# Kernel optimization log

Measured on AMD Instinct MI355X. Metric: run time of the kernel, lower is better.

The kernel has to match this reference:

```python
import jax, jax.numpy as jnp
import numpy as np

B, T, C, H = 4, 2048, 1024, 16
D = C // H  # head dim = 64


def setup_inputs() -> dict:
    key = jax.random.key(0)
    k1, k2, k3 = jax.random.split(key, 3)
    scale = 0.02
    x = jax.random.normal(k1, (B, T, C), dtype=jnp.float32)
    Wqkv = jax.random.normal(k2, (C, 3 * C), dtype=jnp.float32) * scale
    bqkv = jnp.zeros((3 * C,), dtype=jnp.float32)
    Wproj = jax.random.normal(k3, (C, C), dtype=jnp.float32) * scale
    bproj = jnp.zeros((C,), dtype=jnp.float32)
    return {"x": x, "Wqkv": Wqkv, "bqkv": bqkv, "Wproj": Wproj, "bproj": bproj}


def reference(x, Wqkv, bqkv, Wproj, bproj):
    Bx, Tx, Cx = x.shape
    qkv = x @ Wqkv + bqkv  # [B,T,3C]
    q, k, v = jnp.split(qkv, 3, axis=2)
    # [B,T,C] -> [B,H,T,D]
    q = q.reshape(Bx, Tx, H, D).transpose(0, 2, 1, 3)
    k = k.reshape(Bx, Tx, H, D).transpose(0, 2, 1, 3)
    v = v.reshape(Bx, Tx, H, D).transpose(0, 2, 1, 3)
    scores = jnp.einsum('bhqd,bhkd->bhqk', q, k) * (D ** -0.5)
    causal = jnp.tril(jnp.ones((Tx, Tx), dtype=bool))
    scores = jnp.where(causal[None, None], scores, -jnp.inf)
    attn = jax.nn.softmax(scores, axis=-1)
    out = jnp.einsum('bhqk,bhkd->bhqd', attn, v)  # [B,H,T,D]
    out = out.transpose(0, 2, 1, 3).reshape(Bx, Tx, Cx)
    return out @ Wproj + bproj
```

## Files before the change

### kernel.cpp

```cpp
#include <hip/hip_runtime.h>
#include <stdint.h>

typedef __bf16 bf16x8 __attribute__((ext_vector_type(8)));
typedef float  f32x4  __attribute__((ext_vector_type(4)));
typedef short  s16x8  __attribute__((ext_vector_type(8)));

__device__ __forceinline__ unsigned short f2bf(float f) {
  unsigned u = __builtin_bit_cast(unsigned, f);
  u += 0x7fffu + ((u >> 16) & 1u);
  return (unsigned short)(u >> 16);
}

__device__ __forceinline__ bf16x8 ld8(const unsigned short* p) {
  return __builtin_bit_cast(bf16x8, *reinterpret_cast<const s16x8*>(p));
}

#define BB 4
#define TT 2048
#define CC 1024
#define HH 16
#define DD 64
#define MM (BB*TT)

__global__ __launch_bounds__(256) void cvt_f32_bf16(const float* __restrict__ in,
                                                    unsigned short* __restrict__ out, int n) {
  int idx = blockIdx.x * blockDim.x + threadIdx.x;
  int stride = gridDim.x * blockDim.x;
  for (int i = idx * 4; i < n; i += stride * 4) {
    float4 v = *reinterpret_cast<const float4*>(in + i);
    ushort4 o;
    o.x = f2bf(v.x); o.y = f2bf(v.y); o.z = f2bf(v.z); o.w = f2bf(v.w);
    *reinterpret_cast<ushort4*>(out + i) = o;
  }
}

__global__ __launch_bounds__(256) void transpose_cvt(const float* __restrict__ in,
                                                     unsigned short* __restrict__ out,
                                                     int K, int N) {
  __shared__ float tile[32][33];
  int kb = blockIdx.y * 32, nb = blockIdx.x * 32;
  int tx = threadIdx.x, ty = threadIdx.y;
  for (int i = 0; i < 4; i++)
    tile[ty + i*8][tx] = in[(size_t)(kb + ty + i*8) * N + nb + tx];
  __syncthreads();
  for (int i = 0; i < 4; i++)
    out[(size_t)(nb + ty + i*8) * K + kb + tx] = f2bf(tile[tx][ty + i*8]);
}

#define BMT 128
#define BNT 128
#define BKT 32
#define LDT 56

template<int EPI>
__global__ __launch_bounds__(256)
void gemm_bt(const unsigned short* __restrict__ A, const unsigned short* __restrict__ Bt,
             const float* __restrict__ bias, int K,
             unsigned short* __restrict__ qbuf, unsigned short* __restrict__ kbuf,
             unsigned short* __restrict__ vtbuf, float* __restrict__ outf)
{
  __shared__ unsigned short As[BMT * LDT];
  __shared__ unsigned short Bs[BNT * LDT];
  const int tid  = threadIdx.x;
  const int lane = tid & 63;
  const int w    = tid >> 6;
  const int wr   = w >> 1, wc = w & 1;
  const int lo   = lane & 15, hi = lane >> 4;
  const int row0 = blockIdx.x * BMT, col0 = blockIdx.y * BNT;

  f32x4 acc[4][4];
  for (int m = 0; m < 4; m++)
    for (int n = 0; n < 4; n++)
      for (int j = 0; j < 4; j++) acc[m][n][j] = 0.f;

  const int sr = tid >> 2;
  const int sc = (tid & 3) * 8;

  for (int k0 = 0; k0 < K; k0 += BKT) {
    s16x8 a0 = *reinterpret_cast<const s16x8*>(A  + (size_t)(row0 + sr)      * K + k0 + sc);
    s16x8 a1 = *reinterpret_cast<const s16x8*>(A  + (size_t)(row0 + sr + 64) * K + k0 + sc);
    s16x8 b0 = *reinterpret_cast<const s16x8*>(Bt + (size_t)(col0 + sr)      * K + k0 + sc);
    s16x8 b1 = *reinterpret_cast<const s16x8*>(Bt + (size_t)(col0 + sr + 64) * K + k0 + sc);
    *reinterpret_cast<s16x8*>(As + sr        * LDT + sc) = a0;
    *reinterpret_cast<s16x8*>(As + (sr + 64) * LDT + sc) = a1;
    *reinterpret_cast<s16x8*>(Bs + sr        * LDT + sc) = b0;
    *reinterpret_cast<s16x8*>(Bs + (sr + 64) * LDT + sc) = b1;
    __syncthreads();

    bf16x8 af[4], bfr[4];
    for (int m = 0; m < 4; m++)
      af[m] = __builtin_bit_cast(bf16x8,
        *reinterpret_cast<const s16x8*>(As + (wr*64 + m*16 + lo) * LDT + hi*8));
    for (int n = 0; n < 4; n++)
      bfr[n] = __builtin_bit_cast(bf16x8,
        *reinterpret_cast<const s16x8*>(Bs + (wc*64 + n*16 + lo) * LDT + hi*8));
    for (int m = 0; m < 4; m++)
      for (int n = 0; n < 4; n++)
        acc[m][n] = __builtin_amdgcn_mfma_f32_16x16x32_bf16(af[m], bfr[n], acc[m][n], 0, 0, 0);
    __syncthreads();
  }

  if (EPI == 0) {
    const int sec = col0 >> 10;
    for (int m = 0; m < 4; m++) {
      int rbase = row0 + wr*64 + m*16 + hi*4;
      for (int n = 0; n < 4; n++) {
        int c  = col0 + wc*64 + n*16 + lo;
        int cc = c & 1023;
        int h  = cc >> 6, d = cc & 63;
        float bv = bias[c];
        for (int i = 0; i < 4; i++) {
          int r = rbase + i;
          int b = r >> 11, t = r & 2047;
          int bh = b * HH + h;
          unsigned short val = f2bf(acc[m][n][i] + bv);
          if (sec == 0)      qbuf [((size_t)bh * TT + t) * DD + d] = val;
          else if (sec == 1) kbuf [((size_t)bh * TT + t) * DD + d] = val;
          else               vtbuf[((size_t)bh * DD + d) * TT + t] = val;
        }
      }
    }
  } else {
    for (int m = 0; m < 4; m++) {
      int rbase = row0 + wr*64 + m*16 + hi*4;
      for (int n = 0; n < 4; n++) {
        int c = col0 + wc*64 + n*16 + lo;
        float bv = bias[c];
        for (int i = 0; i < 4; i++)
          outf[(size_t)(rbase + i) * CC + c] = acc[m][n][i] + bv;
      }
    }
  }
}

#define PLD 88

__global__ __launch_bounds__(256)
void attn_kernel(const unsigned short* __restrict__ qbuf,
                 const unsigned short* __restrict__ kbuf,
                 const unsigned short* __restrict__ vtbuf,
                 unsigned short* __restrict__ obuf)
{
  __shared__ unsigned short P[4][32 * PLD];
  const int tid  = threadIdx.x;
  const int lane = tid & 63;
  const int w    = tid >> 6;
  const int lo   = lane & 15, hi = lane >> 4;
  const int bh   = blockIdx.x;
  const int qblk = gridDim.y - 1 - blockIdx.y;
  const int qbase = qblk * 128 + w * 32;

  bf16x8 aq[2][2];
  #pragma unroll
  for (int st = 0; st < 2; st++) {
    const unsigned short* qp = qbuf + ((size_t)bh * TT + qbase + st*16 + lo) * DD + hi * 8;
    aq[st][0] = ld8(qp);
    aq[st][1] = ld8(qp + 32);
  }

  float mrow[2][4], lrow[2][4];
  f32x4 acc_o[2][4];
  #pragma unroll
  for (int st = 0; st < 2; st++)
    for (int i = 0; i < 4; i++) {
      mrow[st][i] = -1e30f; lrow[st][i] = 0.f;
      for (int f = 0; f < 4; f++) acc_o[st][f][i] = 0.f;
    }

  unsigned short* Pw = &P[w][0];
  const int nfull = qbase >> 6;

  for (int kt = 0; kt <= nfull; ++kt) {
    const int kbase = kt * 64;
    const bool diag = (kt == nfull);

    f32x4 s[2][4];
    #pragma unroll
    for (int st = 0; st < 2; st++)
      for (int f = 0; f < 4; f++)
        for (int j = 0; j < 4; j++) s[st][f][j] = 0.f;

    __builtin_amdgcn_s_setprio(1);
    #pragma unroll
    for (int f = 0; f < 4; f++) {
      const unsigned short* kp = kbuf + ((size_t)bh * TT + kbase + f*16 + lo) * DD + hi * 8;
      bf16x8 b0 = ld8(kp);
      bf16x8 b1 = ld8(kp + 32);
      s[0][f] = __builtin_amdgcn_mfma_f32_16x16x32_bf16(aq[0][0], b0, s[0][f], 0, 0, 0);
      s[0][f] = __builtin_amdgcn_mfma_f32_16x16x32_bf16(aq[0][1], b1, s[0][f], 0, 0, 0);
      s[1][f] = __builtin_amdgcn_mfma_f32_16x16x32_bf16(aq[1][0], b0, s[1][f], 0, 0, 0);
      s[1][f] = __builtin_amdgcn_mfma_f32_16x16x32_bf16(aq[1][1], b1, s[1][f], 0, 0, 0);
    }
    __builtin_amdgcn_s_setprio(0);

    #pragma unroll
    for (int st = 0; st < 2; st++) {
      const int rowoff = qbase + st*16 + hi*4;
      float tm[4] = {-1e30f, -1e30f, -1e30f, -1e30f};
      #pragma unroll
      for (int f = 0; f < 4; f++)
        for (int i = 0; i < 4; i++) {
          float v = s[st][f][i] * 0.125f;
          if (diag && (kbase + f*16 + lo > rowoff + i)) v = -1e30f;
          s[st][f][i] = v;
          tm[i] = fmaxf(tm[i], v);
        }
      #pragma unroll
      for (int xm = 1; xm < 16; xm <<= 1)
        for (int i = 0; i < 4; i++) tm[i] = fmaxf(tm[i], __shfl_xor(tm[i], xm));
      float rs[4];
      #pragma unroll
      for (int i = 0; i < 4; i++) {
        float mn   = fmaxf(mrow[st][i], tm[i]);
        float corr = __expf(mrow[st][i] - mn);
        mrow[st][i] = mn;
        float r = 0.f;
        #pragma unroll
        for (int f = 0; f < 4; f++) {
          float p = __expf(s[st][f][i] - mn);
          r += p;
          Pw[(st*16 + hi*4 + i) * PLD + f*16 + lo] = f2bf(p);
        }
        rs[i] = r;
        lrow[st][i] *= corr;
        #pragma unroll
        for (int f = 0; f < 4; f++) acc_o[st][f][i] *= corr;
      }
      #pragma unroll
      for (int xm = 1; xm < 16; xm <<= 1)
        for (int i = 0; i < 4; i++) rs[i] += __shfl_xor(rs[i], xm);
      for (int i = 0; i < 4; i++) lrow[st][i] += rs[i];
    }

    bf16x8 pa[2][2];
    #pragma unroll
    for (int st = 0; st < 2; st++) {
      pa[st][0] = ld8(Pw + (st*16 + lo) * PLD + hi * 8);
      pa[st][1] = ld8(Pw + (st*16 + lo) * PLD + 32 + hi * 8);
    }
    __builtin_amdgcn_s_setprio(1);
    #pragma unroll
    for (int f = 0; f < 4; f++) {
      const unsigned short* vp = vtbuf + ((size_t)bh * DD + f*16 + lo) * TT + kbase + hi * 8;
      bf16x8 v0 = ld8(vp);
      bf16x8 v1 = ld8(vp + 32);
      acc_o[0][f] = __builtin_amdgcn_mfma_f32_16x16x32_bf16(pa[0][0], v0, acc_o[0][f], 0, 0, 0);
      acc_o[0][f] = __builtin_amdgcn_mfma_f32_16x16x32_bf16(pa[0][1], v1, acc_o[0][f], 0, 0, 0);
      acc_o[1][f] = __builtin_amdgcn_mfma_f32_16x16x32_bf16(pa[1][0], v0, acc_o[1][f], 0, 0, 0);
      acc_o[1][f] = __builtin_amdgcn_mfma_f32_16x16x32_bf16(pa[1][1], v1, acc_o[1][f], 0, 0, 0);
    }
    __builtin_amdgcn_s_setprio(0);
  }

  const int b = bh >> 4, h = bh & 15;
  #pragma unroll
  for (int st = 0; st < 2; st++)
    for (int f = 0; f < 4; f++)
      for (int i = 0; i < 4; i++) {
        int r = qbase + st*16 + hi*4 + i;
        float v = acc_o[st][f][i] / lrow[st][i];
        obuf[((size_t)(b * TT + r)) * CC + h*64 + f*16 + lo] = f2bf(v);
      }
}

extern "C" void kernel_launch(void* const* d_in, const int* in_sizes, int n_in,
                              void* d_out, int out_size, void* d_ws, size_t ws_size,
                              hipStream_t stream) {
  const float* x     = (const float*)d_in[0];
  const float* Wqkv  = (const float*)d_in[1];
  const float* bqkv  = (const float*)d_in[2];
  const float* Wproj = (const float*)d_in[3];
  const float* bproj = (const float*)d_in[4];
  float* out = (float*)d_out;

  unsigned short* ws  = (unsigned short*)d_ws;
  unsigned short* xb  = ws;
  unsigned short* w1t = xb  + (size_t)MM * CC;
  unsigned short* w2t = w1t + (size_t)3 * CC * CC;
  unsigned short* qbf = w2t + (size_t)CC * CC;
  unsigned short* kbf = qbf + (size_t)BB * HH * TT * DD;
  unsigned short* vtb = kbf + (size_t)BB * HH * TT * DD;
  unsigned short* obf = xb;

  cvt_f32_bf16<<<2048, 256, 0, stream>>>(x, xb, MM * CC);
  transpose_cvt<<<dim3(3*CC/32, CC/32), dim3(32, 8), 0, stream>>>(Wqkv, w1t, CC, 3*CC);
  transpose_cvt<<<dim3(CC/32,  CC/32), dim3(32, 8), 0, stream>>>(Wproj, w2t, CC, CC);

  gemm_bt<0><<<dim3(MM/BMT, 3*CC/BNT), 256, 0, stream>>>(xb, w1t, bqkv, CC,
                                                         qbf, kbf, vtb, nullptr);
  attn_kernel<<<dim3(BB*HH, TT/128), 256, 0, stream>>>(qbf, kbf, vtb, obf);
  gemm_bt<1><<<dim3(MM/BMT, CC/BNT), 256, 0, stream>>>(obf, w2t, bproj, CC,
                                                       nullptr, nullptr, nullptr, out);
}
```

Measured before the change: 371.3 us.

## Use direct global-to-LDS loads in GEMMs and software-pipeline attention QK with PV

The GEMM now loads tiles with global_load_lds straight into unpadded shared memory, skipping the register round-trip. The cost is possible LDS bank conflicts, since the stride drops from 56 to 32. The attention loop computes the next tile's QK scores before the current tile's PV, so score MFMAs overlap softmax and V loads, at the cost of more registers. Softmax folds log2(e) into the scale and uses exp2f instead of __expf.

```diff
diff --git a/kernel.cpp b/kernel.cpp
--- a/kernel.cpp
+++ b/kernel.cpp
@@ -14,6 +14,8 @@
 __device__ __forceinline__ bf16x8 ld8(const unsigned short* p) {
   return __builtin_bit_cast(bf16x8, *reinterpret_cast<const s16x8*>(p));
 }
+
+#define MFMA16(a,b,c) __builtin_amdgcn_mfma_f32_16x16x32_bf16((a),(b),(c),0,0,0)
 
 #define BB 4
 #define TT 2048
@@ -47,68 +49,74 @@
     out[(size_t)(nb + ty + i*8) * K + kb + tx] = f2bf(tile[tx][ty + i*8]);
 }
 
-#define BMT 128
-#define BNT 128
-#define BKT 32
-#define LDT 56
-
 template<int EPI>
 __global__ __launch_bounds__(256)
-void gemm_bt(const unsigned short* __restrict__ A, const unsigned short* __restrict__ Bt,
-             const float* __restrict__ bias, int K,
-             unsigned short* __restrict__ qbuf, unsigned short* __restrict__ kbuf,
-             unsigned short* __restrict__ vtbuf, float* __restrict__ outf)
+void gemm_glds(const unsigned short* __restrict__ A, const unsigned short* __restrict__ Bt,
+               const float* __restrict__ bias, int K,
+               unsigned short* __restrict__ qbuf, unsigned short* __restrict__ kbuf,
+               unsigned short* __restrict__ vtbuf, float* __restrict__ outf)
 {
-  __shared__ unsigned short As[BMT * LDT];
-  __shared__ unsigned short Bs[BNT * LDT];
+  __shared__ __attribute__((aligned(16))) unsigned short As[128 * 32];
+  __shared__ __attribute__((aligned(16))) unsigned short Bs[128 * 32];
   const int tid  = threadIdx.x;
   const int lane = tid & 63;
   const int w    = tid >> 6;
   const int wr   = w >> 1, wc = w & 1;
   const int lo   = lane & 15, hi = lane >> 4;
-  const int row0 = blockIdx.x * BMT, col0 = blockIdx.y * BNT;
+  const int row0 = blockIdx.x * 128, col0 = blockIdx.y * 128;
 
   f32x4 acc[4][4];
+  #pragma unroll
   for (int m = 0; m < 4; m++)
     for (int n = 0; n < 4; n++)
       for (int j = 0; j < 4; j++) acc[m][n][j] = 0.f;
 
-  const int sr = tid >> 2;
-  const int sc = (tid & 3) * 8;
-
-  for (int k0 = 0; k0 < K; k0 += BKT) {
-    s16x8 a0 = *reinterpret_cast<const s16x8*>(A  + (size_t)(row0 + sr)      * K + k0 + sc);
-    s16x8 a1 = *reinterpret_cast<const s16x8*>(A  + (size_t)(row0 + sr + 64) * K + k0 + sc);
-    s16x8 b0 = *reinterpret_cast<const s16x8*>(Bt + (size_t)(col0 + sr)      * K + k0 + sc);
-    s16x8 b1 = *reinterpret_cast<const s16x8*>(Bt + (size_t)(col0 + sr + 64) * K + k0 + sc);
-    *reinterpret_cast<s16x8*>(As + sr        * LDT + sc) = a0;
-    *reinterpret_cast<s16x8*>(As + (sr + 64) * LDT + sc) = a1;
-    *reinterpret_cast<s16x8*>(Bs + sr        * LDT + sc) = b0;
-    *reinterpret_cast<s16x8*>(Bs + (sr + 64) * LDT + sc) = b1;
+  const int srow = lane >> 2;
+  const int scol = (lane & 3) * 8;
+  const unsigned short* Ab = A  + (size_t)(row0 + w*16 + srow) * K + scol;
+  const unsigned short* Bb = Bt + (size_t)(col0 + w*16 + srow) * K + scol;
+  unsigned short* AsW = As + (w*16) * 32;
+  unsigned short* BsW = Bs + (w*16) * 32;
+
+  for (int k0 = 0; k0 < K; k0 += 32) {
     __syncthreads();
+    #pragma unroll
+    for (int i = 0; i < 2; i++) {
+      __builtin_amdgcn_global_load_lds(
+        (const __attribute__((address_space(1))) unsigned int*)(Ab + (size_t)(i*64) * K + k0),
+        (__attribute__((address_space(3))) unsigned int*)(AsW + i*64*32), 16, 0, 0);
+      __builtin_amdgcn_global_load_lds(
+        (const __attribute__((address_space(1))) unsigned int*)(Bb + (size_t)(i*64) * K + k0),
+        (__attribute__((address_space(3))) unsigned int*)(BsW + i*64*32), 16, 0, 0);
+    }
+    __syncthreads();
 
     bf16x8 af[4], bfr[4];
+    #pragma unroll
     for (int m = 0; m < 4; m++)
-      af[m] = __builtin_bit_cast(bf16x8,
-        *reinterpret_cast<const s16x8*>(As + (wr*64 + m*16 + lo) * LDT + hi*8));
+      af[m] = ld8(As + (wr*64 + m*16 + lo) * 32 + hi*8);
+    #pragma unroll
     for (int n = 0; n < 4; n++)
-      bfr[n] = __builtin_bit_cast(bf16x8,
-        *reinterpret_cast<const s16x8*>(Bs + (wc*64 + n*16 + lo) * LDT + hi*8));
+      bfr[n] = ld8(Bs + (wc*64 + n*16 + lo) * 32 + hi*8);
+    #pragma unroll
     for (int m = 0; m < 4; m++)
+      #pragma unroll
       for (int n = 0; n < 4; n++)
-        acc[m][n] = __builtin_amdgcn_mfma_f32_16x16x32_bf16(af[m], bfr[n], acc[m][n], 0, 0, 0);
-    __syncthreads();
+        acc[m][n] = MFMA16(af[m], bfr[n], acc[m][n]);
   }
 
   if (EPI == 0) {
     const int sec = col0 >> 10;
+    #pragma unroll
     for (int m = 0; m < 4; m++) {
       int rbase = row0 + wr*64 + m*16 + hi*4;
+      #pragma unroll
       for (int n = 0; n < 4; n++) {
         int c  = col0 + wc*64 + n*16 + lo;
         int cc = c & 1023;
         int h  = cc >> 6, d = cc & 63;
         float bv = bias[c];
+        #pragma unroll
         for (int i = 0; i < 4; i++) {
           int r = rbase + i;
           int b = r >> 11, t = r & 2047;
@@ -121,11 +129,14 @@
       }
     }
   } else {
+    #pragma unroll
     for (int m = 0; m < 4; m++) {
       int rbase = row0 + wr*64 + m*16 + hi*4;
+      #pragma unroll
       for (int n = 0; n < 4; n++) {
         int c = col0 + wc*64 + n*16 + lo;
         float bv = bias[c];
+        #pragma unroll
         for (int i = 0; i < 4; i++)
           outf[(size_t)(rbase + i) * CC + c] = acc[m][n][i] + bv;
       }
@@ -149,6 +160,10 @@
   const int bh   = blockIdx.x;
   const int qblk = gridDim.y - 1 - blockIdx.y;
   const int qbase = qblk * 128 + w * 32;
+  const float SCL = 0.125f * 1.44269504088896f;
+
+  const unsigned short* Kb = kbuf  + (size_t)bh * TT * DD;
+  const unsigned short* Vb = vtbuf + (size_t)bh * DD * TT;
 
   bf16x8 aq[2][2];
   #pragma unroll
@@ -170,29 +185,26 @@
   unsigned short* Pw = &P[w][0];
   const int nfull = qbase >> 6;
 
-  for (int kt = 0; kt <= nfull; ++kt) {
-    const int kbase = kt * 64;
-    const bool diag = (kt == nfull);
-
-    f32x4 s[2][4];
+  auto QK = [&](int kb2, f32x4 (&so)[2][4]) {
     #pragma unroll
     for (int st = 0; st < 2; st++)
       for (int f = 0; f < 4; f++)
-        for (int j = 0; j < 4; j++) s[st][f][j] = 0.f;
-
+        for (int j = 0; j < 4; j++) so[st][f][j] = 0.f;
     __builtin_amdgcn_s_setprio(1);
     #pragma unroll
     for (int f = 0; f < 4; f++) {
-      const unsigned short* kp = kbuf + ((size_t)bh * TT + kbase + f*16 + lo) * DD + hi * 8;
+      const unsigned short* kp = Kb + (size_t)(kb2 + f*16 + lo) * DD + hi * 8;
       bf16x8 b0 = ld8(kp);
       bf16x8 b1 = ld8(kp + 32);
-      s[0][f] = __builtin_amdgcn_mfma_f32_16x16x32_bf16(aq[0][0], b0, s[0][f], 0, 0, 0);
-      s[0][f] = __builtin_amdgcn_mfma_f32_16x16x32_bf16(aq[0][1], b1, s[0][f], 0, 0, 0);
-      s[1][f] = __builtin_amdgcn_mfma_f32_16x16x32_bf16(aq[1][0], b0, s[1][f], 0, 0, 0);
-      s[1][f] = __builtin_amdgcn_mfma_f32_16x16x32_bf16(aq[1][1], b1, s[1][f], 0, 0, 0);
+      so[0][f] = MFMA16(aq[0][0], b0, so[0][f]);
+      so[0][f] = MFMA16(aq[0][1], b1, so[0][f]);
+      so[1][f] = MFMA16(aq[1][0], b0, so[1][f]);
+      so[1][f] = MFMA16(aq[1][1], b1, so[1][f]);
     }
     __builtin_amdgcn_s_setprio(0);
-
+  };
+
+  auto SM = [&](f32x4 (&sv)[2][4], int kbase, bool diag) {
     #pragma unroll
     for (int st = 0; st < 2; st++) {
       const int rowoff = qbase + st*16 + hi*4;
@@ -200,9 +212,9 @@
       #pragma unroll
       for (int f = 0; f < 4; f++)
         for (int i = 0; i < 4; i++) {
-          float v = s[st][f][i] * 0.125f;
+          float v = sv[st][f][i] * SCL;
           if (diag && (kbase + f*16 + lo > rowoff + i)) v = -1e30f;
-          s[st][f][i] = v;
+          sv[st][f][i] = v;
           tm[i] = fmaxf(tm[i], v);
         }
       #pragma unroll
@@ -212,12 +224,12 @@
       #pragma unroll
       for (int i = 0; i < 4; i++) {
         float mn   = fmaxf(mrow[st][i], tm[i]);
-        float corr = __expf(mrow[st][i] - mn);
+        float corr = exp2f(mrow[st][i] - mn);
         mrow[st][i] = mn;
         float r = 0.f;
         #pragma unroll
         for (int f = 0; f < 4; f++) {
-          float p = __expf(s[st][f][i] - mn);
+          float p = exp2f(sv[st][f][i] - mn);
           r += p;
           Pw[(st*16 + hi*4 + i) * PLD + f*16 + lo] = f2bf(p);
         }
@@ -231,7 +243,9 @@
         for (int i = 0; i < 4; i++) rs[i] += __shfl_xor(rs[i], xm);
       for (int i = 0; i < 4; i++) lrow[st][i] += rs[i];
     }
-
+  };
+
+  auto PV = [&](int kbase) {
     bf16x8 pa[2][2];
     #pragma unroll
     for (int st = 0; st < 2; st++) {
@@ -241,16 +255,31 @@
     __builtin_amdgcn_s_setprio(1);
     #pragma unroll
     for (int f = 0; f < 4; f++) {
-      const unsigned short* vp = vtbuf + ((size_t)bh * DD + f*16 + lo) * TT + kbase + hi * 8;
+      const unsigned short* vp = Vb + (size_t)(f*16 + lo) * TT + kbase + hi * 8;
       bf16x8 v0 = ld8(vp);
       bf16x8 v1 = ld8(vp + 32);
-      acc_o[0][f] = __builtin_amdgcn_mfma_f32_16x16x32_bf16(pa[0][0], v0, acc_o[0][f], 0, 0, 0);
-      acc_o[0][f] = __builtin_amdgcn_mfma_f32_16x16x32_bf16(pa[0][1], v1, acc_o[0][f], 0, 0, 0);
-      acc_o[1][f] = __builtin_amdgcn_mfma_f32_16x16x32_bf16(pa[1][0], v0, acc_o[1][f], 0, 0, 0);
-      acc_o[1][f] = __builtin_amdgcn_mfma_f32_16x16x32_bf16(pa[1][1], v1, acc_o[1][f], 0, 0, 0);
+      acc_o[0][f] = MFMA16(pa[0][0], v0, acc_o[0][f]);
+      acc_o[0][f] = MFMA16(pa[0][1], v1, acc_o[0][f]);
+      acc_o[1][f] = MFMA16(pa[1][0], v0, acc_o[1][f]);
+      acc_o[1][f] = MFMA16(pa[1][1], v1, acc_o[1][f]);
     }
     __builtin_amdgcn_s_setprio(0);
-  }
+  };
+
+  f32x4 s[2][4];
+  QK(0, s);
+  for (int kt = 0; kt < nfull; ++kt) {
+    SM(s, kt*64, false);
+    f32x4 sn[2][4];
+    QK((kt+1)*64, sn);
+    PV(kt*64);
+    #pragma unroll
+    for (int st = 0; st < 2; st++)
+      for (int f = 0; f < 4; f++)
+        s[st][f] = sn[st][f];
+  }
+  SM(s, nfull*64, true);
+  PV(nfull*64);
 
   const int b = bh >> 4, h = bh & 15;
   #pragma unroll
@@ -286,9 +315,9 @@
   transpose_cvt<<<dim3(3*CC/32, CC/32), dim3(32, 8), 0, stream>>>(Wqkv, w1t, CC, 3*CC);
   transpose_cvt<<<dim3(CC/32,  CC/32), dim3(32, 8), 0, stream>>>(Wproj, w2t, CC, CC);
 
-  gemm_bt<0><<<dim3(MM/BMT, 3*CC/BNT), 256, 0, stream>>>(xb, w1t, bqkv, CC,
-                                                         qbf, kbf, vtb, nullptr);
+  gemm_glds<0><<<dim3(MM/128, 3*CC/128), 256, 0, stream>>>(xb, w1t, bqkv, CC,
+                                                           qbf, kbf, vtb, nullptr);
   attn_kernel<<<dim3(BB*HH, TT/128), 256, 0, stream>>>(qbf, kbf, vtb, obf);
-  gemm_bt<1><<<dim3(MM/BMT, CC/BNT), 256, 0, stream>>>(obf, w2t, bproj, CC,
-                                                       nullptr, nullptr, nullptr, out);
-}
+  gemm_glds<1><<<dim3(MM/128, CC/128), 256, 0, stream>>>(obf, w2t, bproj, CC,
+                                                         nullptr, nullptr, nullptr, out);
+}
```

Measured after the change: 453.4 us. 1.22x slower.
